# Performance work log

Hardware: AMD Instinct MI355X
Metric: run time of the kernel (lower is better)

The kernel has to match this reference:

```python
import jax, jax.numpy as jnp
import numpy as np

ALPHA = 0.01
EPS = 1e-7
B, C, D = 64, 1501, 2048


def setup_inputs() -> dict:
    key = jax.random.key(0)
    k1, k2, k3 = jax.random.split(key, 3)
    x = jax.random.normal(k1, (B, D), dtype=jnp.float32)
    cls_list = jax.random.randint(k2, (B,), 0, C, dtype=jnp.int64)
    memory = jax.random.normal(k3, (C, D), dtype=jnp.float32)
    return {"x": x, "cls_list": cls_list, "memory": memory}


def reference(x, cls_list, memory):
    # selected_cls_weights: gather of ORIGINAL memory rows (read happens before
    # the scatter in the torch loop, since the loop writes tmp_memory, not memory)
    selected = memory[cls_list]                      # [B, D]
    tmp_memory = memory.at[cls_list].set(x)          # [C, D]
    # EMA update + row-wise L2 normalize (side-effect state in torch; returned here for checking)
    new_mem = memory * (1.0 - ALPHA) + tmp_memory * ALPHA
    new_mem = new_mem / (jnp.linalg.norm(new_mem, axis=1, keepdims=True) + EPS)
    # torch does tmp_memory.repeat(B,1,1); broadcast expresses the same values
    tmp_repeated = jnp.broadcast_to(tmp_memory[None], (x.shape[0], C, D))  # [B, C, D]
    return (selected, tmp_repeated, new_mem)
```

## Files before the change

### kernel.cpp

```cpp
#include <hip/hip_runtime.h>
#include <math.h>


#define ALPHA 0.01f
#define EPS_  1e-7f
#define B_    64
#define C_    1501
#define D_    2048
#define T_    256

typedef float f32x4 __attribute__((ext_vector_type(4)));

__global__ __launch_bounds__(T_) void memorybank_kernel(
    const float* __restrict__ x,
    const int*   __restrict__ cls,
    const float* __restrict__ mem,
    float*       __restrict__ out)
{
    const int c   = blockIdx.x;
    const int tid = threadIdx.x;

    __shared__ unsigned long long s_mask;
    if (tid < 64) {
        int cb = cls[tid];
        unsigned long long m = __ballot(cb == c);
        if (tid == 0) s_mask = m;
    }
    __syncthreads();
    const unsigned long long mask = s_mask;
    const int winner = mask ? (63 - __clzll(mask)) : -1;

    const f32x4* mrow = (const f32x4*)(mem + (size_t)c * D_);
    f32x4 m0 = mrow[tid];
    f32x4 m1 = mrow[tid + T_];

    f32x4 t0 = m0, t1 = m1;
    if (winner >= 0) {
        const f32x4* xrow = (const f32x4*)(x + (size_t)winner * D_);
        t0 = xrow[tid];
        t1 = xrow[tid + T_];
    }

    f32x4 n0 = m0 * (1.0f - ALPHA) + t0 * ALPHA;
    f32x4 n1 = m1 * (1.0f - ALPHA) + t1 * ALPHA;

    float ss = n0.x*n0.x + n0.y*n0.y + n0.z*n0.z + n0.w*n0.w
             + n1.x*n1.x + n1.y*n1.y + n1.z*n1.z + n1.w*n1.w;
    #pragma unroll
    for (int off = 32; off > 0; off >>= 1)
        ss += __shfl_xor(ss, off, 64);
    __shared__ float s_part[T_ / 64];
    if ((tid & 63) == 0) s_part[tid >> 6] = ss;
    __syncthreads();
    const float total = s_part[0] + s_part[1] + s_part[2] + s_part[3];
    const float inv = 1.0f / (sqrtf(total) + EPS_);

    f32x4* out_sel = (f32x4*)out;
    f32x4* out_rep = (f32x4*)(out + (size_t)B_ * D_);
    f32x4* out_new = (f32x4*)(out + (size_t)B_ * D_ + (size_t)B_ * C_ * D_);

    {
        f32x4 w0 = n0 * inv;
        f32x4 w1 = n1 * inv;
        const size_t base = (size_t)c * (D_ / 4);
        out_new[base + tid]      = w0;
        out_new[base + tid + T_] = w1;
    }

    unsigned long long mm = mask;
    while (mm) {
        const int b = __ffsll(mm) - 1;
        mm &= mm - 1;
        const size_t base = (size_t)b * (D_ / 4);
        out_sel[base + tid]      = m0;
        out_sel[base + tid + T_] = m1;
    }

    const size_t rowbase = (size_t)c * (D_ / 4) + tid;
    const size_t strideB = (size_t)C_ * (D_ / 4);
    #pragma unroll 4
    for (int b = 0; b < B_; ++b) {
        __builtin_nontemporal_store(t0, &out_rep[rowbase + (size_t)b * strideB]);
        __builtin_nontemporal_store(t1, &out_rep[rowbase + (size_t)b * strideB + T_]);
    }
}

extern "C" void kernel_launch(void* const* d_in, const int* in_sizes, int n_in,
                              void* d_out, int out_size, void* d_ws, size_t ws_size,
                              hipStream_t stream) {
    const float* x   = (const float*)d_in[0];
    const int*   cls = (const int*)  d_in[1];
    const float* mem = (const float*)d_in[2];
    float*       out = (float*)d_out;
    memorybank_kernel<<<C_, T_, 0, stream>>>(x, cls, mem, out);
}
```

Baseline: 779.4 us.

## Split replication into a separate 2D-grid kernel to spread broadcast writes

The single kernel is split into a prep kernel, which computes the EMA, the normalization and the gathers and writes slice 0 of the repeated output, and a replicate kernel. The replicate kernel runs on a 1501x9 grid, reads slice 0 back and writes 7 copies per block. This targets the serialized 64-iteration store loop per block by spreading the broadcast writes over many more blocks for better parallelism. It costs an extra launch and a read-back of slice 0, and it drops the nontemporal store hints.

Result: no change. 785.4 us (+0.8%).

```diff
diff --git a/kernel.cpp b/kernel.cpp
--- a/kernel.cpp
+++ b/kernel.cpp
@@ -8,10 +8,12 @@
 #define C_    1501
 #define D_    2048
 #define T_    256
+#define REP_PER_BLK 7
+#define REP_GRID_Y  9
 
 typedef float f32x4 __attribute__((ext_vector_type(4)));
 
-__global__ __launch_bounds__(T_) void memorybank_kernel(
+__global__ __launch_bounds__(T_) void mb_prep(
     const float* __restrict__ x,
     const int*   __restrict__ cls,
     const float* __restrict__ mem,
@@ -59,13 +61,13 @@
     f32x4* out_rep = (f32x4*)(out + (size_t)B_ * D_);
     f32x4* out_new = (f32x4*)(out + (size_t)B_ * D_ + (size_t)B_ * C_ * D_);
 
-    {
-        f32x4 w0 = n0 * inv;
-        f32x4 w1 = n1 * inv;
-        const size_t base = (size_t)c * (D_ / 4);
-        out_new[base + tid]      = w0;
-        out_new[base + tid + T_] = w1;
-    }
+    const size_t rbase = (size_t)c * (D_ / 4);
+
+    out_rep[rbase + tid]      = t0;
+    out_rep[rbase + tid + T_] = t1;
+
+    out_new[rbase + tid]      = n0 * inv;
+    out_new[rbase + tid + T_] = n1 * inv;
 
     unsigned long long mm = mask;
     while (mm) {
@@ -75,13 +77,27 @@
         out_sel[base + tid]      = m0;
         out_sel[base + tid + T_] = m1;
     }
+}
 
-    const size_t rowbase = (size_t)c * (D_ / 4) + tid;
-    const size_t strideB = (size_t)C_ * (D_ / 4);
-    #pragma unroll 4
-    for (int b = 0; b < B_; ++b) {
-        __builtin_nontemporal_store(t0, &out_rep[rowbase + (size_t)b * strideB]);
-        __builtin_nontemporal_store(t1, &out_rep[rowbase + (size_t)b * strideB + T_]);
+__global__ __launch_bounds__(T_) void mb_replicate(float* __restrict__ out)
+{
+    const int c   = blockIdx.x;
+    const int by  = blockIdx.y;
+    const int tid = threadIdx.x;
+
+    f32x4* rep = (f32x4*)(out + (size_t)B_ * D_);
+    const size_t slab  = (size_t)C_ * (D_ / 4);
+    const size_t rbase = (size_t)c * (D_ / 4);
+
+    f32x4 v0 = rep[rbase + tid];
+    f32x4 v1 = rep[rbase + tid + T_];
+
+    const int b0 = 1 + by * REP_PER_BLK;
+    #pragma unroll
+    for (int k = 0; k < REP_PER_BLK; ++k) {
+        const size_t dst = (size_t)(b0 + k) * slab + rbase;
+        rep[dst + tid]      = v0;
+        rep[dst + tid + T_] = v1;
     }
 }
 
@@ -92,5 +108,7 @@
     const int*   cls = (const int*)  d_in[1];
     const float* mem = (const float*)d_in[2];
     float*       out = (float*)d_out;
-    memorybank_kernel<<<C_, T_, 0, stream>>>(x, cls, mem, out);
+
+    mb_prep<<<C_, T_, 0, stream>>>(x, cls, mem, out);
+    mb_replicate<<<dim3(C_, REP_GRID_Y), T_, 0, stream>>>(out);
 }
```
